# Optimization experiments

Hardware: AMD Instinct MI355X
Metric: run time of the kernel (lower is better)

## Reference

```python
import jax, jax.numpy as jnp
import numpy as np

EPS = 1e-08


def setup_inputs() -> dict:
    key = jax.random.key(0)
    k_in, k_style, k_w = jax.random.split(key, 3)
    B, I, O, K, H, W = 4, 64, 64, 3, 512, 512
    inp = jax.random.normal(k_in, (B, I, H, W), dtype=jnp.float32)
    style = jax.random.normal(k_style, (B, I), dtype=jnp.float32)
    # Equalized init: weight ~ N(0,1) scaled by 1/sqrt(fan_in), fan_in = I*K*K
    w_scale = 1.0 / np.sqrt(I * K * K)
    weight = w_scale * jax.random.normal(k_w, (O, I, K, K), dtype=jnp.float32)
    return {"input": inp, "style": style, "weight": weight}


def reference(input, style, weight):
    # input: (B, I, H, W); style: (B, I); weight: (O, I, K, K)
    B, I, H, W = input.shape
    O, _, K, _ = weight.shape
    # style modulation -> per-sample weights (B, O, I, K, K)
    w = weight[None] * style[:, None, :, None, None]
    # demodulation: normalize each (sample, out-channel) filter
    sigma = jnp.sqrt(EPS + jnp.sum(w * w, axis=(2, 3, 4), keepdims=True))
    w = w / sigma
    # grouped conv with groups = B (one group per sample)
    w = w.reshape(B * O, I, K, K)
    x = input.reshape(1, B * I, H, W)
    pad = (K - 1) // 2
    out = jax.lax.conv_general_dilated(
        x, w,
        window_strides=(1, 1),
        padding=[(pad, pad), (pad, pad)],
        dimension_numbers=("NCHW", "OIHW", "NCHW"),
        feature_group_count=B,
    )
    return out.reshape(B, O, H, W)
```

## Files before the change

kernel.cpp:

```cpp
#include <hip/hip_runtime.h>
#include <hip/hip_bf16.h>

#define HW 512
#define IC 64
#define OC 64
#define NB 4

#define SROW 66
#define CPR (SROW * 8)
#define NCHUNK (6 * CPR)

typedef short s16x8 __attribute__((ext_vector_type(8)));
typedef float f32x16 __attribute__((ext_vector_type(16)));

__global__ __launch_bounds__(64) void demod_kernel(
    const float* __restrict__ weight,
    const float* __restrict__ style,
    __hip_bfloat16* __restrict__ wd)
{
    const int bo = blockIdx.x;
    const int b = bo >> 6;
    const int o = bo & 63;
    const int i = threadIdx.x;

    const float st = style[b * IC + i];
    float v[9];
    float s = 0.f;
#pragma unroll
    for (int t = 0; t < 9; ++t) {
        const float w = weight[(o * IC + i) * 9 + t] * st;
        v[t] = w;
        s += w * w;
    }
#pragma unroll
    for (int off = 32; off >= 1; off >>= 1) s += __shfl_xor(s, off);
    const float rs = 1.0f / sqrtf(1e-8f + s);
#pragma unroll
    for (int t = 0; t < 9; ++t)
        wd[(((b * 9 + t) * 8 + (i >> 3)) * OC + o) * 8 + (i & 7)] =
            __float2bfloat16(v[t] * rs);
}

__global__ __launch_bounds__(256) void nchw_to_nhwc_bf16(
    const float* __restrict__ in,
    __hip_bfloat16* __restrict__ t)
{
    __shared__ unsigned short lds[64 * 130];
    const int tid = threadIdx.x;
    const int xb = blockIdx.x * 128;
    const int y = blockIdx.y;
    const int b = blockIdx.z;

#pragma unroll
    for (int it = 0; it < 8; ++it) {
        const int idx = it * 256 + tid;
        const int i = idx >> 5;
        const int xq = idx & 31;
        const float4 v = *(const float4*)(in +
            (((long)(b * IC + i) * HW + y) * HW + xb + xq * 4));
        __hip_bfloat16 h0 = __float2bfloat16(v.x), h1 = __float2bfloat16(v.y);
        __hip_bfloat16 h2 = __float2bfloat16(v.z), h3 = __float2bfloat16(v.w);
        unsigned p01 = ((unsigned)*(unsigned short*)&h1 << 16) | *(unsigned short*)&h0;
        unsigned p23 = ((unsigned)*(unsigned short*)&h3 << 16) | *(unsigned short*)&h2;
        *(unsigned*)&lds[i * 130 + xq * 4] = p01;
        *(unsigned*)&lds[i * 130 + xq * 4 + 2] = p23;
    }
    __syncthreads();
    unsigned short* tp = (unsigned short*)t;
#pragma unroll
    for (int it = 0; it < 4; ++it) {
        const int idx = it * 256 + tid;
        const int x = idx >> 3;
        const int g = idx & 7;
        unsigned r[4];
#pragma unroll
        for (int cp = 0; cp < 4; ++cp) {
            unsigned lo = lds[(g * 8 + cp * 2) * 130 + x];
            unsigned hi = lds[(g * 8 + cp * 2 + 1) * 130 + x];
            r[cp] = (hi << 16) | lo;
        }
        uint4 o4 = {r[0], r[1], r[2], r[3]};
        *(uint4*)(tp + (((long)(b * HW + y) * HW + xb + x) * IC + g * 8)) = o4;
    }
}

__device__ __forceinline__ void gload_lds16(const void* g, void* l) {
    __builtin_amdgcn_global_load_lds(
        (const __attribute__((address_space(1))) unsigned*)(unsigned long long)g,
        (__attribute__((address_space(3))) unsigned*)(unsigned)(unsigned long long)l,
        16, 0, 0);
}

__global__ __launch_bounds__(256, 3) void conv_mfma(
    const __hip_bfloat16* __restrict__ tin,
    const __hip_bfloat16* __restrict__ wd,
    float* __restrict__ out)
{
    __shared__ __align__(16) unsigned short bin[NCHUNK * 8];

    const int tid = threadIdx.x;
    const int wave = tid >> 6, lane = tid & 63;
    const int l31 = lane & 31, hi = lane >> 5;

    const int id = blockIdx.x;
    const int xcd = id & 7, slot = id >> 3;
    const int b = xcd >> 1;
    const int xb = (slot & 7) << 6;
    const int ybase = ((xcd & 1) << 8) | ((slot >> 3) << 2);

    const unsigned short* tb = (const unsigned short*)tin + (long)b * HW * HW * IC;
    const unsigned short* wp = (const unsigned short*)wd + b * 9 * 8 * OC * 8;

#pragma unroll
    for (int it = 0; it < 13; ++it) {
        const int n = (it == 12) ? (NCHUNK - 256 + tid) : (it * 256 + tid);
        const int r = n / CPR;
        const int q = n - r * CPR;
        const int px = q >> 3, sl = q & 7;
        const int cg = sl ^ (px & 7);
        int xg = xb + px - 1; xg = xg < 0 ? 0 : (xg > HW - 1 ? HW - 1 : xg);
        int yg = ybase + r - 1; yg = yg < 0 ? 0 : (yg > HW - 1 ? HW - 1 : yg);
        const unsigned short* src = tb + ((long)yg * HW + xg) * IC + cg * 8;
        gload_lds16(src, &bin[n * 8]);
    }
    __syncthreads();

    if (ybase == 0 || ybase == HW - 4 || xb == 0 || xb == HW - 64) {
        const uint4 z = {0u, 0u, 0u, 0u};
        if (ybase == 0) {
#pragma unroll
            for (int k = 0; k < 3; ++k) {
                const int q = k * 256 + tid;
                if (q < CPR) *(uint4*)&bin[q * 8] = z;
            }
        }
        if (ybase == HW - 4) {
#pragma unroll
            for (int k = 0; k < 3; ++k) {
                const int q = k * 256 + tid;
                if (q < CPR) *(uint4*)&bin[(5 * CPR + q) * 8] = z;
            }
        }
        if (xb == 0 && tid < 48)
            *(uint4*)&bin[((tid >> 3) * CPR + (tid & 7)) * 8] = z;
        if (xb == HW - 64 && tid < 48)
            *(uint4*)&bin[((tid >> 3) * CPR + 65 * 8 + (tid & 7)) * 8] = z;
        __syncthreads();
    }

    f32x16 acc[2][2];
#pragma unroll
    for (int mt = 0; mt < 2; ++mt)
#pragma unroll
        for (int nt = 0; nt < 2; ++nt)
#pragma unroll
            for (int e = 0; e < 16; ++e) acc[mt][nt][e] = 0.f;

#pragma unroll
    for (int ky = 0; ky < 3; ++ky) {
        const int rr = (wave + ky) * SROW;
#pragma unroll
        for (int kx = 0; kx < 3; ++kx) {
            const int tap = ky * 3 + kx;
            const int e7 = (l31 + kx) & 7;
#pragma unroll
            for (int ks = 0; ks < 4; ++ks) {
                const int cg = ks * 2 + hi;
                const int sl = cg ^ e7;
                s16x8 af[2], bf[2];
#pragma unroll
                for (int mt = 0; mt < 2; ++mt)
                    af[mt] = *(const s16x8*)(wp + (tap * 8 + cg) * 512 +
                                             (mt * 32 + l31) * 8);
#pragma unroll
                for (int nt = 0; nt < 2; ++nt) {
                    const int s = nt * 32 + l31 + kx;
                    bf[nt] = *(const s16x8*)(&bin[((rr + s) * 8 + sl) * 8]);
                }
#pragma unroll
                for (int mt = 0; mt < 2; ++mt)
#pragma unroll
                    for (int nt = 0; nt < 2; ++nt)
                        acc[mt][nt] = __builtin_amdgcn_mfma_f32_32x32x16_bf16(
                            af[mt], bf[nt], acc[mt][nt], 0, 0, 0);
            }
        }
    }

    const int y = ybase + wave;
#pragma unroll
    for (int mt = 0; mt < 2; ++mt) {
#pragma unroll
        for (int g = 0; g < 4; ++g) {
#pragma unroll
            for (int r = 0; r < 4; ++r) {
                const int o = mt * 32 + r + g * 8 + hi * 4;
                float* orow = out + ((long)(b * OC + o) * HW + y) * HW + xb;
#pragma unroll
                for (int nt = 0; nt < 2; ++nt)
                    orow[nt * 32 + l31] = acc[mt][nt][g * 4 + r];
            }
        }
    }
}

extern "C" void kernel_launch(void* const* d_in, const int* in_sizes, int n_in,
                              void* d_out, int out_size, void* d_ws, size_t ws_size,
                              hipStream_t stream) {
    const float* inp = (const float*)d_in[0];
    const float* style = (const float*)d_in[1];
    const float* weight = (const float*)d_in[2];
    float* out = (float*)d_out;

    __hip_bfloat16* wd = (__hip_bfloat16*)d_ws;
    __hip_bfloat16* tin = (__hip_bfloat16*)((char*)d_ws + 0x60000);

    demod_kernel<<<dim3(NB * OC), dim3(64), 0, stream>>>(weight, style, wd);
    nchw_to_nhwc_bf16<<<dim3(HW / 128, HW, NB), dim3(256), 0, stream>>>(inp, tin);
    conv_mfma<<<dim3(NB * HW * 2), dim3(256), 0, stream>>>(tin, wd, out);
}
```

Baseline: 540.9 us.

## Fuse NCHW-to-NHWC bf16 conversion into conv tile loading

Removes the separate transpose/convert kernel and its bf16 workspace round-trip. The conv kernel now loads fp32 NCHW rows directly, converts them to bf16 and writes them into the swizzled LDS tile. Halo columns are fetched with scalar loads, and out-of-range rows are zero-filled inline. This cuts global traffic and one launch, but the conv now reads fp32, which is twice the bytes per halo-overlapped tile, and its loads are no longer asynchronous direct-to-LDS.

```diff
diff --git a/kernel.cpp b/kernel.cpp
--- a/kernel.cpp
+++ b/kernel.cpp
@@ -7,8 +7,6 @@
 #define NB 4
 
 #define SROW 66
-#define CPR (SROW * 8)
-#define NCHUNK (6 * CPR)
 
 typedef short s16x8 __attribute__((ext_vector_type(8)));
 typedef float f32x16 __attribute__((ext_vector_type(16)));
@@ -41,62 +39,20 @@
             __float2bfloat16(v[t] * rs);
 }
 
-__global__ __launch_bounds__(256) void nchw_to_nhwc_bf16(
-    const float* __restrict__ in,
-    __hip_bfloat16* __restrict__ t)
-{
-    __shared__ unsigned short lds[64 * 130];
-    const int tid = threadIdx.x;
-    const int xb = blockIdx.x * 128;
-    const int y = blockIdx.y;
-    const int b = blockIdx.z;
-
-#pragma unroll
-    for (int it = 0; it < 8; ++it) {
-        const int idx = it * 256 + tid;
-        const int i = idx >> 5;
-        const int xq = idx & 31;
-        const float4 v = *(const float4*)(in +
-            (((long)(b * IC + i) * HW + y) * HW + xb + xq * 4));
-        __hip_bfloat16 h0 = __float2bfloat16(v.x), h1 = __float2bfloat16(v.y);
-        __hip_bfloat16 h2 = __float2bfloat16(v.z), h3 = __float2bfloat16(v.w);
-        unsigned p01 = ((unsigned)*(unsigned short*)&h1 << 16) | *(unsigned short*)&h0;
-        unsigned p23 = ((unsigned)*(unsigned short*)&h3 << 16) | *(unsigned short*)&h2;
-        *(unsigned*)&lds[i * 130 + xq * 4] = p01;
-        *(unsigned*)&lds[i * 130 + xq * 4 + 2] = p23;
-    }
-    __syncthreads();
-    unsigned short* tp = (unsigned short*)t;
-#pragma unroll
-    for (int it = 0; it < 4; ++it) {
-        const int idx = it * 256 + tid;
-        const int x = idx >> 3;
-        const int g = idx & 7;
-        unsigned r[4];
-#pragma unroll
-        for (int cp = 0; cp < 4; ++cp) {
-            unsigned lo = lds[(g * 8 + cp * 2) * 130 + x];
-            unsigned hi = lds[(g * 8 + cp * 2 + 1) * 130 + x];
-            r[cp] = (hi << 16) | lo;
-        }
-        uint4 o4 = {r[0], r[1], r[2], r[3]};
-        *(uint4*)(tp + (((long)(b * HW + y) * HW + xb + x) * IC + g * 8)) = o4;
-    }
+static __device__ __forceinline__ unsigned short bf16_bits(float f) {
+    __hip_bfloat16 h = __float2bfloat16(f);
+    return *(unsigned short*)&h;
 }
-
-__device__ __forceinline__ void gload_lds16(const void* g, void* l) {
-    __builtin_amdgcn_global_load_lds(
-        (const __attribute__((address_space(1))) unsigned*)(unsigned long long)g,
-        (__attribute__((address_space(3))) unsigned*)(unsigned)(unsigned long long)l,
-        16, 0, 0);
+static __device__ __forceinline__ unsigned pack2(float lo, float hi) {
+    return ((unsigned)bf16_bits(hi) << 16) | (unsigned)bf16_bits(lo);
 }
 
 __global__ __launch_bounds__(256, 3) void conv_mfma(
-    const __hip_bfloat16* __restrict__ tin,
+    const float* __restrict__ in,
     const __hip_bfloat16* __restrict__ wd,
     float* __restrict__ out)
 {
-    __shared__ __align__(16) unsigned short bin[NCHUNK * 8];
+    __shared__ __align__(16) unsigned short bin[6 * SROW * 8 * 8];
 
     const int tid = threadIdx.x;
     const int wave = tid >> 6, lane = tid & 63;
@@ -108,45 +64,63 @@
     const int xb = (slot & 7) << 6;
     const int ybase = ((xcd & 1) << 8) | ((slot >> 3) << 2);
 
-    const unsigned short* tb = (const unsigned short*)tin + (long)b * HW * HW * IC;
+    const float* ib = in + (long)b * IC * HW * HW;
     const unsigned short* wp = (const unsigned short*)wd + b * 9 * 8 * OC * 8;
 
+    {
+        const int g = lane >> 2;
+        const int qi = lane & 3;
 #pragma unroll
-    for (int it = 0; it < 13; ++it) {
-        const int n = (it == 12) ? (NCHUNK - 256 + tid) : (it * 256 + tid);
-        const int r = n / CPR;
-        const int q = n - r * CPR;
-        const int px = q >> 3, sl = q & 7;
-        const int cg = sl ^ (px & 7);
-        int xg = xb + px - 1; xg = xg < 0 ? 0 : (xg > HW - 1 ? HW - 1 : xg);
-        int yg = ybase + r - 1; yg = yg < 0 ? 0 : (yg > HW - 1 ? HW - 1 : yg);
-        const unsigned short* src = tb + ((long)yg * HW + xg) * IC + cg * 8;
-        gload_lds16(src, &bin[n * 8]);
+        for (int it = 0; it < 3; ++it) {
+            const int idx = it * 4 + wave;
+            const int r = idx >> 1;
+            const int q = ((idx & 1) << 2) | qi;
+            const int yg = ybase + r - 1;
+            float4 v[8];
+            if ((unsigned)yg < (unsigned)HW) {
+                const float* src = ib + ((long)(q * 8) * HW + yg) * HW + xb + g * 4;
+#pragma unroll
+                for (int c = 0; c < 8; ++c)
+                    v[c] = *(const float4*)(src + (long)c * HW * HW);
+            } else {
+#pragma unroll
+                for (int c = 0; c < 8; ++c) v[c] = make_float4(0.f, 0.f, 0.f, 0.f);
+            }
+#pragma unroll
+            for (int j = 0; j < 4; ++j) {
+                const int px = g * 4 + 1 + j;
+                const int sl = q ^ (px & 7);
+                float e[8];
+#pragma unroll
+                for (int c = 0; c < 8; ++c)
+                    e[c] = (j == 0) ? v[c].x : (j == 1) ? v[c].y
+                         : (j == 2) ? v[c].z : v[c].w;
+                uint4 o4 = { pack2(e[0], e[1]), pack2(e[2], e[3]),
+                             pack2(e[4], e[5]), pack2(e[6], e[7]) };
+                *(uint4*)&bin[((r * SROW + px) * 8 + sl) * 8] = o4;
+            }
+        }
+    }
+    if (tid < 96) {
+        const int e_ = tid & 1;
+        const int rq = tid >> 1;
+        const int r = rq >> 3, q = rq & 7;
+        const int x = e_ ? (xb + 64) : (xb - 1);
+        const int yg = ybase + r - 1;
+        const bool ok = ((unsigned)x < (unsigned)HW) & ((unsigned)yg < (unsigned)HW);
+        float f[8];
+#pragma unroll
+        for (int c = 0; c < 8; ++c) {
+            f[c] = 0.f;
+            if (ok) f[c] = ib[((long)(q * 8 + c) * HW + yg) * HW + x];
+        }
+        const int px = e_ ? 65 : 0;
+        const int sl = q ^ (px & 7);
+        uint4 o4 = { pack2(f[0], f[1]), pack2(f[2], f[3]),
+                     pack2(f[4], f[5]), pack2(f[6], f[7]) };
+        *(uint4*)&bin[((r * SROW + px) * 8 + sl) * 8] = o4;
     }
     __syncthreads();
-
-    if (ybase == 0 || ybase == HW - 4 || xb == 0 || xb == HW - 64) {
-        const uint4 z = {0u, 0u, 0u, 0u};
-        if (ybase == 0) {
-#pragma unroll
-            for (int k = 0; k < 3; ++k) {
-                const int q = k * 256 + tid;
-                if (q < CPR) *(uint4*)&bin[q * 8] = z;
-            }
-        }
-        if (ybase == HW - 4) {
-#pragma unroll
-            for (int k = 0; k < 3; ++k) {
-                const int q = k * 256 + tid;
-                if (q < CPR) *(uint4*)&bin[(5 * CPR + q) * 8] = z;
-            }
-        }
-        if (xb == 0 && tid < 48)
-            *(uint4*)&bin[((tid >> 3) * CPR + (tid & 7)) * 8] = z;
-        if (xb == HW - 64 && tid < 48)
-            *(uint4*)&bin[((tid >> 3) * CPR + 65 * 8 + (tid & 7)) * 8] = z;
-        __syncthreads();
-    }
 
     f32x16 acc[2][2];
 #pragma unroll
@@ -213,9 +187,7 @@
     float* out = (float*)d_out;
 
     __hip_bfloat16* wd = (__hip_bfloat16*)d_ws;
-    __hip_bfloat16* tin = (__hip_bfloat16*)((char*)d_ws + 0x60000);
 
     demod_kernel<<<dim3(NB * OC), dim3(64), 0, stream>>>(weight, style, wd);
-    nchw_to_nhwc_bf16<<<dim3(HW / 128, HW, NB), dim3(256), 0, stream>>>(inp, tin);
-    conv_mfma<<<dim3(NB * HW * 2), dim3(256), 0, stream>>>(tin, wd, out);
+    conv_mfma<<<dim3(NB * HW * 2), dim3(256), 0, stream>>>(inp, wd, out);
 }
```

After: 499.0 us. -7.8%, faster.
